# Kernel optimization log

Hardware: AMD Instinct MI355X
Metric: run time of the kernel (lower is better)

## Reference

```python
import jax, jax.numpy as jnp
import numpy as np

K = 4096      # codebook_size
D = 256       # emb_dim
DECAY = 0.99
EPS = 1e-05
BETA = 0.25


def setup_inputs() -> dict:
    key = jax.random.key(0)
    k1, k2 = jax.random.split(key)
    z_e = jax.random.normal(k1, (32, 1024, D), dtype=jnp.float32)
    codebook = jax.random.normal(k2, (K, D), dtype=jnp.float32) * 0.05
    ema_cluster_size = jnp.zeros((K,), dtype=jnp.float32)
    ema_embed_sum = jnp.zeros((K, D), dtype=jnp.float32)
    return {"z_e": z_e, "codebook": codebook,
            "ema_cluster_size": ema_cluster_size,
            "ema_embed_sum": ema_embed_sum}


def reference(z_e, codebook, ema_cluster_size, ema_embed_sum):
    lead_shape = z_e.shape[:-1]
    z = z_e.reshape(-1, D)                       # [N, D]
    N = z.shape[0]

    # squared distances: ||z||^2 + ||e||^2 - 2 z e^T   -> [N, K]
    z_sq = jnp.sum(z * z, axis=1, keepdims=True)
    e_sq = jnp.sum(codebook * codebook, axis=1)
    distances = z_sq + e_sq[None, :] - 2.0 * (z @ codebook.T)
    indices = jnp.argmin(distances, axis=1)      # [N]

    z_q = codebook[indices].reshape(z_e.shape)   # gather

    commitment = jnp.mean((z_e - jax.lax.stop_gradient(z_q)) ** 2)
    loss_vq = BETA * commitment
    z_q_st = z_e + jax.lax.stop_gradient(z_q - z_e)  # straight-through

    # EMA statistics (scatter-reduce instead of dense one-hot matmul)
    cluster_size_batch = jax.ops.segment_sum(
        jnp.ones((N,), dtype=z.dtype), indices, num_segments=K)
    embed_sum_batch = jax.ops.segment_sum(z, indices, num_segments=K)

    new_ema_cluster_size = ema_cluster_size * DECAY + (1.0 - DECAY) * cluster_size_batch
    new_ema_embed_sum = ema_embed_sum * DECAY + (1.0 - DECAY) * embed_sum_batch
    n = new_ema_cluster_size + EPS * K
    new_codebook = new_ema_embed_sum / n[:, None]

    avg_probs = cluster_size_batch / N
    perplexity = jnp.exp(-jnp.sum(avg_probs * jnp.log(avg_probs + 1e-12)))

    return (z_q_st, indices.reshape(lead_shape), loss_vq, perplexity,
            new_codebook, new_ema_cluster_size, new_ema_embed_sum)
```

## Files before the change

### kernel.cpp

```cpp
#include <hip/hip_runtime.h>
#include <hip/hip_bf16.h>
#include <math.h>

#define DIM    256
#define KCB    4096
#define NROWS  32768
#define DECAYF 0.99f
#define MARGIN 0.024f

#define OUT_ZQ   0
#define OUT_IDX  8388608
#define OUT_LOSS 8421376
#define OUT_PPL  8421377
#define OUT_CB   8421378
#define OUT_CS   9469954
#define OUT_ES   9474050

#define WS_A2      0u
#define WS_EH      33554432u
#define WS_ZSQ     35651584u
#define WS_ESQ     35782656u
#define WS_P1      35799040u
#define WS_PI      39993344u
#define WS_P2      44187648u
#define WS_IDX     48381952u
#define WS_FLIST   48513024u
#define WS_LIST2   48644096u
#define WS_BASE    48775168u
#define WS_ZERO    48791552u
#define WS_COUNTS  48791552u
#define WS_CURSOR  48807936u
#define WS_FLCNT   48824320u
#define WS_ZEROLEN 32772u

#define WS_SLOT    WS_A2
#define WS_CBT     (WS_A2 + 1048576u)

typedef __attribute__((ext_vector_type(8))) short short8;
typedef __attribute__((ext_vector_type(4))) float f32x4;

#define GLOAD(g, l) __builtin_amdgcn_global_load_lds( \
    (const __attribute__((address_space(1))) unsigned int*)(g), \
    (__attribute__((address_space(3))) unsigned int*)(l), 16, 0, 0)

__device__ __forceinline__ unsigned short f2bf(float x) {
  __hip_bfloat16 h = __float2bfloat16(x);
  return *reinterpret_cast<unsigned short*>(&h);
}

__global__ __launch_bounds__(256) void prep_all(
    const float* __restrict__ z, const float* __restrict__ cb,
    unsigned short* __restrict__ A2, unsigned short* __restrict__ EH,
    float* __restrict__ z_sq, float* __restrict__ e_sq) {
  int b = blockIdx.x;
  int lane = threadIdx.x & 63;
  const float* src;
  unsigned short* dst;
  float* sq;
  int gw;
  if (b < NROWS / 4) {
    gw = (b * 256 + threadIdx.x) >> 6;
    src = z; dst = A2; sq = z_sq;
  } else {
    gw = ((b - NROWS / 4) * 256 + threadIdx.x) >> 6;
    src = cb; dst = EH; sq = e_sq;
  }
  float4 v = *(const float4*)(src + (size_t)gw * DIM + lane * 4);
  float x[4] = {v.x, v.y, v.z, v.w};
  unsigned short h[4];
  float ss = 0.f;
#pragma unroll
  for (int i = 0; i < 4; ++i) { ss += x[i] * x[i]; h[i] = f2bf(x[i]); }
  *(ushort4*)(dst + (size_t)gw * 256 + lane * 4) =
      make_ushort4(h[0], h[1], h[2], h[3]);
#pragma unroll
  for (int off = 32; off > 0; off >>= 1) ss += __shfl_down(ss, off);
  if (lane == 0) sq[gw] = ss;
}

__global__ __launch_bounds__(256) void tp_cb(
    const float* __restrict__ cb, float* __restrict__ cbT) {
  __shared__ float tile[32][257];
  int c0 = blockIdx.x * 32;
  int t = threadIdx.x;
  int r = t >> 6, c4 = (t & 63) * 4;
#pragma unroll
  for (int i = 0; i < 8; ++i) {
    float4 v = *(const float4*)(cb + (size_t)(c0 + r + i * 4) * DIM + c4);
    tile[r + i * 4][c4 + 0] = v.x;
    tile[r + i * 4][c4 + 1] = v.y;
    tile[r + i * 4][c4 + 2] = v.z;
    tile[r + i * 4][c4 + 3] = v.w;
  }
  __syncthreads();
  int cs = (t & 7) * 4;
#pragma unroll
  for (int j = 0; j < 8; ++j) {
    int d = (t >> 3) + j * 32;
    float4 w = make_float4(tile[cs][d], tile[cs + 1][d],
                           tile[cs + 2][d], tile[cs + 3][d]);
    *(float4*)(cbT + (size_t)d * KCB + c0 + cs) = w;
  }
}

__global__ __launch_bounds__(256) void dist_mfma(
    const unsigned short* __restrict__ A2, const unsigned short* __restrict__ EH,
    const float* __restrict__ e_sq,
    float* __restrict__ p1, int* __restrict__ pi, float* __restrict__ p2) {
  __shared__ __align__(16) unsigned short sZ[3][128 * 32];
  __shared__ __align__(16) unsigned short sE[3][128 * 32];
  __shared__ float se[128];
  __shared__ float sm1[2][128];
  __shared__ int   smi[2][128];
  __shared__ float sm2[2][128];

  int wgid = blockIdx.x;
  int swz = (wgid & 7) * 1024 + (wgid >> 3);
  int rowp = swz >> 5, colp = swz & 31;
  int brow = rowp * 128, bcol = colp * 128;
  int tid = threadIdx.x;
  int lane = tid & 63, w = tid >> 6;
  int wr = w >> 1, wc = w & 1;
  int rl = lane & 15, k8 = lane >> 4;

  f32x4 acc[4][4] = {};

  int r0 = tid >> 2;
  int s_src = (tid & 3) ^ (r0 & 3) ^ ((r0 >> 2) & 3);
  const char* baseA = (const char*)A2 + (size_t)(brow + r0) * 512 + s_src * 16;
  const char* baseB = (const char*)EH + (size_t)(bcol + r0) * 512 + s_src * 16;

#define STAGE(b, ks_) do {                                                    \
    GLOAD(baseA + (ks_) * 64,         &sZ[b][tid * 8]);                       \
    GLOAD(baseA + 32768 + (ks_) * 64, &sZ[b][2048 + tid * 8]);                \
    GLOAD(baseB + (ks_) * 64,         &sE[b][tid * 8]);                       \
    GLOAD(baseB + 32768 + (ks_) * 64, &sE[b][2048 + tid * 8]);                \
  } while (0)

  if (tid < 128) se[tid] = e_sq[bcol + tid];
  STAGE(0, 0);
  STAGE(1, 1);
  __syncthreads();

#pragma unroll
  for (int ks = 0; ks < 8; ++ks) {
    if (ks >= 2 && ks < 7) { asm volatile("s_waitcnt vmcnt(4)" ::: "memory"); }
    if (ks == 7)           { asm volatile("s_waitcnt vmcnt(0)" ::: "memory"); }
    if (ks >= 1) {
      __builtin_amdgcn_sched_barrier(0);
      __builtin_amdgcn_s_barrier();
      __builtin_amdgcn_sched_barrier(0);
    }
    const unsigned short* za = sZ[ks % 3];
    const unsigned short* ea = sE[ks % 3];
    short8 ef[4], zf[4];
    int sseg = (k8 ^ (rl & 3) ^ ((rl >> 2) & 3)) * 8;
#pragma unroll
    for (int mi = 0; mi < 4; ++mi)
      ef[mi] = *(const short8*)&ea[(wr * 64 + mi * 16 + rl) * 32 + sseg];
#pragma unroll
    for (int ni = 0; ni < 4; ++ni)
      zf[ni] = *(const short8*)&za[(wc * 64 + ni * 16 + rl) * 32 + sseg];
#pragma unroll
    for (int mi = 0; mi < 4; ++mi)
#pragma unroll
      for (int ni = 0; ni < 4; ++ni)
        acc[mi][ni] = __builtin_amdgcn_mfma_f32_16x16x32_bf16(
            ef[mi], zf[ni], acc[mi][ni], 0, 0, 0);
    if (ks < 6) STAGE((ks + 2) % 3, ks + 2);
  }
#undef STAGE

  int cb0 = bcol + wr * 64 + k8 * 4;
  float e2l[4][4];
#pragma unroll
  for (int mi = 0; mi < 4; ++mi)
#pragma unroll
    for (int j = 0; j < 4; ++j)
      e2l[mi][j] = se[wr * 64 + mi * 16 + k8 * 4 + j];

#pragma unroll
  for (int ni = 0; ni < 4; ++ni) {
    float m1 = 1e30f, m2 = 1e30f; int i1 = 0;
#pragma unroll
    for (int mi = 0; mi < 4; ++mi) {
#pragma unroll
      for (int j = 0; j < 4; ++j) {
        float q = e2l[mi][j] - 2.0f * acc[mi][ni][j];
        if (q < m1) { m2 = m1; m1 = q; i1 = cb0 + mi * 16 + j; }
        else if (q < m2) m2 = q;
      }
    }
#pragma unroll
    for (int mk = 16; mk <= 32; mk <<= 1) {
      float v1 = __shfl_xor(m1, mk);
      int   vi = __shfl_xor(i1, mk);
      float v2 = __shfl_xor(m2, mk);
      float hi = fmaxf(m1, v1), lo2 = fminf(m2, v2);
      if (v1 < m1) { m1 = v1; i1 = vi; }
      else if (v1 == m1 && vi < i1) i1 = vi;
      m2 = fminf(hi, lo2);
    }
    if (k8 == 0) {
      int rowl = wc * 64 + ni * 16 + rl;
      sm1[wr][rowl] = m1; smi[wr][rowl] = i1; sm2[wr][rowl] = m2;
    }
  }
  __syncthreads();
  if (tid < 128) {
    float a1 = sm1[0][tid]; int ai = smi[0][tid]; float a2 = sm2[0][tid];
    float b1 = sm1[1][tid]; int bi = smi[1][tid]; float b2 = sm2[1][tid];
    float m1, m2; int i1;
    if (b1 < a1) { m1 = b1; i1 = bi; m2 = fminf(a1, b2); }
    else         { m1 = a1; i1 = ai; m2 = fminf(b1, a2); }
    size_t o = (size_t)colp * NROWS + (brow + tid);
    p1[o] = m1; pi[o] = i1; p2[o] = m2;
  }
}

__global__ __launch_bounds__(256) void merge_kernel(
    const float* __restrict__ p1, const int* __restrict__ pi,
    const float* __restrict__ p2, int* __restrict__ flist,
    int* __restrict__ flcnt, unsigned long long* __restrict__ slot) {
  int r = blockIdx.x * 256 + threadIdx.x;
  float m1 = 1e30f, m2 = 1e30f; int i1 = 0;
  for (int cb = 0; cb < 32; ++cb) {
    size_t o = (size_t)cb * NROWS + r;
    float v1 = p1[o]; int vi = pi[o]; float v2 = p2[o];
    float hi = fmaxf(m1, v1), lo2 = fminf(m2, v2);
    if (v1 < m1) { m1 = v1; i1 = vi; }
    else if (v1 == m1 && vi < i1) i1 = vi;
    m2 = fminf(hi, lo2);
  }
  if (m2 - m1 < MARGIN) {
    slot[r] = ~0ULL;
    int p = atomicAdd(flcnt, 1);
    flist[p] = r;
  } else {
    slot[r] = ((unsigned long long)__float_as_uint(m1) << 32) | (unsigned)i1;
  }
}

__global__ __launch_bounds__(256) void rescore_partial(
    const float* __restrict__ z, const float* __restrict__ cbT,
    const float* __restrict__ z_sq, const float* __restrict__ e_sq,
    const int* __restrict__ flist, const int* __restrict__ flcnt,
    unsigned long long* __restrict__ slot) {
  __shared__ float zs[8][256];
  __shared__ int   rid[8];
  __shared__ float zq[8];
  __shared__ unsigned long long wred[4][8];
  int t = threadIdx.x;
  int lane = t & 63, w = t >> 6;
  int cnt = *flcnt;
  int nitems = ((cnt + 7) >> 3) << 2;
  for (int it = blockIdx.x; it < nitems; it += gridDim.x) {
    int batch = it >> 2, quarter = it & 3;
    __syncthreads();
    if (t < 8) {
      int fi = batch * 8 + t;
      int rr = flist[fi < cnt ? fi : (cnt - 1)];
      rid[t] = rr; zq[t] = z_sq[rr];
    }
    __syncthreads();
    {
      int r8 = t >> 5, d0 = (t & 31) * 8;
      const float* zp = z + (size_t)rid[r8] * DIM + d0;
      *(float4*)&zs[r8][d0] = *(const float4*)(zp);
      *(float4*)&zs[r8][d0 + 4] = *(const float4*)(zp + 4);
    }
    __syncthreads();
    int cbase = quarter * 1024 + t * 4;
    float4 es4 = *(const float4*)(e_sq + cbase);
    float a0[8], a1[8], a2[8], a3[8];
#pragma unroll
    for (int r = 0; r < 8; ++r) { a0[r] = 0.f; a1[r] = 0.f; a2[r] = 0.f; a3[r] = 0.f; }
    for (int d = 0; d < DIM; ++d) {
      float4 e = *(const float4*)(cbT + (size_t)d * KCB + cbase);
#pragma unroll
      for (int r = 0; r < 8; ++r) {
        float zv = zs[r][d];
        a0[r] = fmaf(zv, e.x, a0[r]);
        a1[r] = fmaf(zv, e.y, a1[r]);
        a2[r] = fmaf(zv, e.z, a2[r]);
        a3[r] = fmaf(zv, e.w, a3[r]);
      }
    }
#pragma unroll
    for (int r = 0; r < 8; ++r) {
      float d0 = (zq[r] + es4.x) - 2.0f * a0[r];
      float d1 = (zq[r] + es4.y) - 2.0f * a1[r];
      float d2 = (zq[r] + es4.z) - 2.0f * a2[r];
      float d3 = (zq[r] + es4.w) - 2.0f * a3[r];
      float m = d0; int ci = cbase;
      if (d1 < m) { m = d1; ci = cbase + 1; }
      if (d2 < m) { m = d2; ci = cbase + 2; }
      if (d3 < m) { m = d3; ci = cbase + 3; }
      unsigned long long p =
          ((unsigned long long)__float_as_uint(m) << 32) | (unsigned)ci;
#pragma unroll
      for (int mk = 32; mk >= 1; mk >>= 1) {
        unsigned long long q = __shfl_xor(p, mk);
        if (q < p) p = q;
      }
      if (lane == 0) wred[w][r] = p;
    }
    __syncthreads();
    if (t < 8) {
      unsigned long long m = wred[0][t];
      if (wred[1][t] < m) m = wred[1][t];
      if (wred[2][t] < m) m = wred[2][t];
      if (wred[3][t] < m) m = wred[3][t];
      atomicMin(&slot[rid[t]], m);
    }
  }
}

__global__ __launch_bounds__(256) void gather_kernel(
    const float* __restrict__ z, const float* __restrict__ cb,
    const unsigned long long* __restrict__ slot, int* __restrict__ idx,
    float* __restrict__ out_idxf, float* __restrict__ out_zq,
    int* __restrict__ counts, float* __restrict__ lossp) {
  __shared__ float ls[4];
  int gw = (blockIdx.x * 256 + threadIdx.x) >> 6;
  int lane = threadIdx.x & 63;
  int w = threadIdx.x >> 6;
  int k = (int)(unsigned)(slot[gw] & 0xFFFFFFFFu);
  float4 zq = *(const float4*)(cb + (size_t)k * DIM + lane * 4);
  float4 zv = *(const float4*)(z + (size_t)gw * DIM + lane * 4);
  float4 o;
  o.x = zv.x + (zq.x - zv.x);
  o.y = zv.y + (zq.y - zv.y);
  o.z = zv.z + (zq.z - zv.z);
  o.w = zv.w + (zq.w - zv.w);
  *(float4*)(out_zq + (size_t)gw * DIM + lane * 4) = o;
  float dx = zv.x - zq.x, dy = zv.y - zq.y, dz = zv.z - zq.z, dw = zv.w - zq.w;
  float s = dx * dx + dy * dy + dz * dz + dw * dw;
#pragma unroll
  for (int off = 32; off > 0; off >>= 1) s += __shfl_down(s, off);
  if (lane == 0) {
    ls[w] = s;
    idx[gw] = k;
    out_idxf[gw] = (float)k;
    atomicAdd(&counts[k], 1);
  }
  __syncthreads();
  if (threadIdx.x == 0)
    lossp[blockIdx.x] = ls[0] + ls[1] + ls[2] + ls[3];
}

__global__ void prefix_kernel(const int* __restrict__ counts,
                              int* __restrict__ base, int* __restrict__ cursor) {
  __shared__ int part[256];
  __shared__ int pre[256];
  int t = threadIdx.x;
  int loc[16]; int s = 0;
#pragma unroll
  for (int i = 0; i < 16; ++i) { loc[i] = counts[t * 16 + i]; s += loc[i]; }
  part[t] = s;
  __syncthreads();
  if (t == 0) { int a = 0; for (int i = 0; i < 256; ++i) { pre[i] = a; a += part[i]; } }
  __syncthreads();
  int a = pre[t];
#pragma unroll
  for (int i = 0; i < 16; ++i) { base[t * 16 + i] = a; cursor[t * 16 + i] = a; a += loc[i]; }
}

__global__ void scatter_kernel(const int* __restrict__ idx,
                               int* __restrict__ cursor, int* __restrict__ list2) {
  int n = blockIdx.x * 256 + threadIdx.x;
  int k = idx[n];
  int p = atomicAdd(&cursor[k], 1);
  list2[p] = n;
}

__global__ __launch_bounds__(256) void finalize_codes(
    const float* __restrict__ ema_cs, const float* __restrict__ ema_es,
    const int* __restrict__ counts, const int* __restrict__ base,
    const int* __restrict__ list2, const float* __restrict__ z,
    float* __restrict__ out_cb, float* __restrict__ out_cs,
    float* __restrict__ out_es, const float* __restrict__ lossp,
    float* __restrict__ out_loss, float* __restrict__ out_ppl) {
  __shared__ float red[256];
  int gw = (blockIdx.x * 256 + threadIdx.x) >> 6;
  int lane = threadIdx.x & 63;
  int cnt = counts[gw], b0 = base[gw];
  float sx = 0.f, sy = 0.f, sz = 0.f, sw = 0.f;
  for (int i = 0; i < cnt; ++i) {
    int n = list2[b0 + i];
    float4 v = *(const float4*)(z + (size_t)n * DIM + lane * 4);
    sx += v.x; sy += v.y; sz += v.z; sw += v.w;
  }
  const float omd = 1.0f - DECAYF;
  float cntf = (float)cnt;
  float ncs = ema_cs[gw] * DECAYF + omd * cntf;
  float nden = ncs + 0.04096f;
  if (lane == 0) out_cs[gw] = ncs;
  size_t o = (size_t)gw * DIM + lane * 4;
  float4 em = *(const float4*)(ema_es + o);
  float nex = em.x * DECAYF + omd * sx;
  float ney = em.y * DECAYF + omd * sy;
  float nez = em.z * DECAYF + omd * sz;
  float new_ = em.w * DECAYF + omd * sw;
  *(float2*)(out_es + o) = make_float2(nex, ney);
  *(float2*)(out_es + o + 2) = make_float2(nez, new_);
  *(float2*)(out_cb + o) = make_float2(nex / nden, ney / nden);
  *(float2*)(out_cb + o + 2) = make_float2(nez / nden, new_ / nden);

  if (blockIdx.x == 0) {
    int t = threadIdx.x;
    float s = 0.f;
    for (int i = t; i < 8192; i += 256) s += lossp[i];
    float e = 0.f;
    for (int i = t; i < 4096; i += 256) {
      float p = (float)counts[i] * (1.0f / (float)NROWS);
      e -= p * logf(p + 1e-12f);
    }
    red[t] = s;
    __syncthreads();
    for (int st = 128; st > 0; st >>= 1) {
      if (t < st) red[t] += red[t + st];
      __syncthreads();
    }
    float loss_tot = red[0];
    __syncthreads();
    red[t] = e;
    __syncthreads();
    for (int st = 128; st > 0; st >>= 1) {
      if (t < st) red[t] += red[t + st];
      __syncthreads();
    }
    if (t == 0) {
      out_loss[0] = 0.25f * (loss_tot / 8388608.0f);
      out_ppl[0] = expf(red[0]);
    }
  }
}

extern "C" void kernel_launch(void* const* d_in, const int* in_sizes, int n_in,
                              void* d_out, int out_size, void* d_ws, size_t ws_size,
                              hipStream_t stream) {
  (void)in_sizes; (void)n_in; (void)out_size; (void)ws_size;
  const float* z      = (const float*)d_in[0];
  const float* cb     = (const float*)d_in[1];
  const float* ema_cs = (const float*)d_in[2];
  const float* ema_es = (const float*)d_in[3];
  float* out = (float*)d_out;
  char*  ws  = (char*)d_ws;

  unsigned short* A2 = (unsigned short*)(ws + WS_A2);
  unsigned short* EH = (unsigned short*)(ws + WS_EH);
  float* z_sq  = (float*)(ws + WS_ZSQ);
  float* e_sq  = (float*)(ws + WS_ESQ);
  float* p1    = (float*)(ws + WS_P1);
  int*   pi    = (int*)(ws + WS_PI);
  float* p2    = (float*)(ws + WS_P2);
  float* lossp = (float*)(ws + WS_P2);
  unsigned long long* slot = (unsigned long long*)(ws + WS_SLOT);
  float* cbT   = (float*)(ws + WS_CBT);
  int*   idx   = (int*)(ws + WS_IDX);
  int*   flist = (int*)(ws + WS_FLIST);
  int*   list2 = (int*)(ws + WS_LIST2);
  int*   base  = (int*)(ws + WS_BASE);
  int*   counts = (int*)(ws + WS_COUNTS);
  int*   cursor = (int*)(ws + WS_CURSOR);
  int*   flcnt  = (int*)(ws + WS_FLCNT);

  hipMemsetAsync(ws + WS_ZERO, 0, WS_ZEROLEN, stream);

  prep_all<<<NROWS / 4 + KCB / 4, 256, 0, stream>>>(z, cb, A2, EH, z_sq, e_sq);
  dist_mfma<<<(NROWS / 128) * (KCB / 128), 256, 0, stream>>>(A2, EH, e_sq,
                                                             p1, pi, p2);
  tp_cb<<<KCB / 32, 256, 0, stream>>>(cb, cbT);
  merge_kernel<<<NROWS / 256, 256, 0, stream>>>(p1, pi, p2, flist, flcnt,
                                                slot);
  rescore_partial<<<2048, 256, 0, stream>>>(z, cbT, z_sq, e_sq, flist, flcnt,
                                            slot);
  gather_kernel<<<NROWS / 4, 256, 0, stream>>>(z, cb, slot, idx,
                                               out + OUT_IDX, out + OUT_ZQ,
                                               counts, lossp);
  prefix_kernel<<<1, 256, 0, stream>>>(counts, base, cursor);
  scatter_kernel<<<NROWS / 256, 256, 0, stream>>>(idx, cursor, list2);
  finalize_codes<<<KCB / 4, 256, 0, stream>>>(ema_cs, ema_es, counts, base,
                                              list2, z, out + OUT_CB,
                                              out + OUT_CS, out + OUT_ES,
                                              lossp, out + OUT_LOSS,
                                              out + OUT_PPL);
}
```

Before: 258.6 us.

## Restage dist GEMM into two four-buffer bulk phases and fuse transpose with merge

The distance GEMM's three-buffer software pipeline, with per-k-step barriers and partial waitcnts, is replaced by two phases. Each phase loads four K-slices into a four-deep LDS buffer, waits for all of them, then runs four MFMA steps back to back. Separately, the codebook transpose kernel is merged into the merge kernel as extra blocks, which removes one launch. The GEMM change cuts barriers but drops load/compute overlap and doubles LDS use, which may lower occupancy.

```diff
diff --git a/kernel.cpp b/kernel.cpp
--- a/kernel.cpp
+++ b/kernel.cpp
@@ -78,37 +78,12 @@
   if (lane == 0) sq[gw] = ss;
 }
 
-__global__ __launch_bounds__(256) void tp_cb(
-    const float* __restrict__ cb, float* __restrict__ cbT) {
-  __shared__ float tile[32][257];
-  int c0 = blockIdx.x * 32;
-  int t = threadIdx.x;
-  int r = t >> 6, c4 = (t & 63) * 4;
-#pragma unroll
-  for (int i = 0; i < 8; ++i) {
-    float4 v = *(const float4*)(cb + (size_t)(c0 + r + i * 4) * DIM + c4);
-    tile[r + i * 4][c4 + 0] = v.x;
-    tile[r + i * 4][c4 + 1] = v.y;
-    tile[r + i * 4][c4 + 2] = v.z;
-    tile[r + i * 4][c4 + 3] = v.w;
-  }
-  __syncthreads();
-  int cs = (t & 7) * 4;
-#pragma unroll
-  for (int j = 0; j < 8; ++j) {
-    int d = (t >> 3) + j * 32;
-    float4 w = make_float4(tile[cs][d], tile[cs + 1][d],
-                           tile[cs + 2][d], tile[cs + 3][d]);
-    *(float4*)(cbT + (size_t)d * KCB + c0 + cs) = w;
-  }
-}
-
 __global__ __launch_bounds__(256) void dist_mfma(
     const unsigned short* __restrict__ A2, const unsigned short* __restrict__ EH,
     const float* __restrict__ e_sq,
     float* __restrict__ p1, int* __restrict__ pi, float* __restrict__ p2) {
-  __shared__ __align__(16) unsigned short sZ[3][128 * 32];
-  __shared__ __align__(16) unsigned short sE[3][128 * 32];
+  __shared__ __align__(16) unsigned short sZ[4][128 * 32];
+  __shared__ __align__(16) unsigned short sE[4][128 * 32];
   __shared__ float se[128];
   __shared__ float sm1[2][128];
   __shared__ int   smi[2][128];
@@ -137,38 +112,40 @@
     GLOAD(baseB + 32768 + (ks_) * 64, &sE[b][2048 + tid * 8]);                \
   } while (0)
 
+#define COMPUTE(bi) do {                                                      \
+    const unsigned short* za = sZ[bi];                                        \
+    const unsigned short* ea = sE[bi];                                        \
+    short8 ef[4], zf[4];                                                      \
+    _Pragma("unroll")                                                         \
+    for (int mi = 0; mi < 4; ++mi)                                            \
+      ef[mi] = *(const short8*)&ea[(wr * 64 + mi * 16 + rl) * 32 + sseg];     \
+    _Pragma("unroll")                                                         \
+    for (int ni = 0; ni < 4; ++ni)                                            \
+      zf[ni] = *(const short8*)&za[(wc * 64 + ni * 16 + rl) * 32 + sseg];     \
+    _Pragma("unroll")                                                         \
+    for (int mi = 0; mi < 4; ++mi)                                            \
+      _Pragma("unroll")                                                       \
+      for (int ni = 0; ni < 4; ++ni)                                          \
+        acc[mi][ni] = __builtin_amdgcn_mfma_f32_16x16x32_bf16(                \
+            ef[mi], zf[ni], acc[mi][ni], 0, 0, 0);                            \
+  } while (0)
+
+  int sseg = (k8 ^ (rl & 3) ^ ((rl >> 2) & 3)) * 8;
+
   if (tid < 128) se[tid] = e_sq[bcol + tid];
-  STAGE(0, 0);
-  STAGE(1, 1);
-  __syncthreads();
-
-#pragma unroll
-  for (int ks = 0; ks < 8; ++ks) {
-    if (ks >= 2 && ks < 7) { asm volatile("s_waitcnt vmcnt(4)" ::: "memory"); }
-    if (ks == 7)           { asm volatile("s_waitcnt vmcnt(0)" ::: "memory"); }
-    if (ks >= 1) {
-      __builtin_amdgcn_sched_barrier(0);
-      __builtin_amdgcn_s_barrier();
-      __builtin_amdgcn_sched_barrier(0);
-    }
-    const unsigned short* za = sZ[ks % 3];
-    const unsigned short* ea = sE[ks % 3];
-    short8 ef[4], zf[4];
-    int sseg = (k8 ^ (rl & 3) ^ ((rl >> 2) & 3)) * 8;
-#pragma unroll
-    for (int mi = 0; mi < 4; ++mi)
-      ef[mi] = *(const short8*)&ea[(wr * 64 + mi * 16 + rl) * 32 + sseg];
-#pragma unroll
-    for (int ni = 0; ni < 4; ++ni)
-      zf[ni] = *(const short8*)&za[(wc * 64 + ni * 16 + rl) * 32 + sseg];
-#pragma unroll
-    for (int mi = 0; mi < 4; ++mi)
-#pragma unroll
-      for (int ni = 0; ni < 4; ++ni)
-        acc[mi][ni] = __builtin_amdgcn_mfma_f32_16x16x32_bf16(
-            ef[mi], zf[ni], acc[mi][ni], 0, 0, 0);
-    if (ks < 6) STAGE((ks + 2) % 3, ks + 2);
-  }
+  STAGE(0, 0); STAGE(1, 1); STAGE(2, 2); STAGE(3, 3);
+  asm volatile("s_waitcnt vmcnt(0)" ::: "memory");
+  __syncthreads();
+
+  COMPUTE(0); COMPUTE(1); COMPUTE(2); COMPUTE(3);
+  __syncthreads();
+
+  STAGE(0, 4); STAGE(1, 5); STAGE(2, 6); STAGE(3, 7);
+  asm volatile("s_waitcnt vmcnt(0)" ::: "memory");
+  __syncthreads();
+
+  COMPUTE(0); COMPUTE(1); COMPUTE(2); COMPUTE(3);
+#undef COMPUTE
 #undef STAGE
 
   int cb0 = bcol + wr * 64 + k8 * 4;
@@ -218,26 +195,52 @@
   }
 }
 
-__global__ __launch_bounds__(256) void merge_kernel(
+__global__ __launch_bounds__(256) void merge_tp(
     const float* __restrict__ p1, const int* __restrict__ pi,
     const float* __restrict__ p2, int* __restrict__ flist,
-    int* __restrict__ flcnt, unsigned long long* __restrict__ slot) {
-  int r = blockIdx.x * 256 + threadIdx.x;
-  float m1 = 1e30f, m2 = 1e30f; int i1 = 0;
-  for (int cb = 0; cb < 32; ++cb) {
-    size_t o = (size_t)cb * NROWS + r;
-    float v1 = p1[o]; int vi = pi[o]; float v2 = p2[o];
-    float hi = fmaxf(m1, v1), lo2 = fminf(m2, v2);
-    if (v1 < m1) { m1 = v1; i1 = vi; }
-    else if (v1 == m1 && vi < i1) i1 = vi;
-    m2 = fminf(hi, lo2);
-  }
-  if (m2 - m1 < MARGIN) {
-    slot[r] = ~0ULL;
-    int p = atomicAdd(flcnt, 1);
-    flist[p] = r;
+    int* __restrict__ flcnt, unsigned long long* __restrict__ slot,
+    const float* __restrict__ cb, float* __restrict__ cbT) {
+  __shared__ float tile[32][257];
+  int b = blockIdx.x;
+  int t = threadIdx.x;
+  if (b < NROWS / 256) {
+    int r = b * 256 + t;
+    float m1 = 1e30f, m2 = 1e30f; int i1 = 0;
+    for (int cbk = 0; cbk < 32; ++cbk) {
+      size_t o = (size_t)cbk * NROWS + r;
+      float v1 = p1[o]; int vi = pi[o]; float v2 = p2[o];
+      float hi = fmaxf(m1, v1), lo2 = fminf(m2, v2);
+      if (v1 < m1) { m1 = v1; i1 = vi; }
+      else if (v1 == m1 && vi < i1) i1 = vi;
+      m2 = fminf(hi, lo2);
+    }
+    if (m2 - m1 < MARGIN) {
+      slot[r] = ~0ULL;
+      int p = atomicAdd(flcnt, 1);
+      flist[p] = r;
+    } else {
+      slot[r] = ((unsigned long long)__float_as_uint(m1) << 32) | (unsigned)i1;
+    }
   } else {
-    slot[r] = ((unsigned long long)__float_as_uint(m1) << 32) | (unsigned)i1;
+    int c0 = (b - NROWS / 256) * 32;
+    int r = t >> 6, c4 = (t & 63) * 4;
+#pragma unroll
+    for (int i = 0; i < 8; ++i) {
+      float4 v = *(const float4*)(cb + (size_t)(c0 + r + i * 4) * DIM + c4);
+      tile[r + i * 4][c4 + 0] = v.x;
+      tile[r + i * 4][c4 + 1] = v.y;
+      tile[r + i * 4][c4 + 2] = v.z;
+      tile[r + i * 4][c4 + 3] = v.w;
+    }
+    __syncthreads();
+    int cs = (t & 7) * 4;
+#pragma unroll
+    for (int j = 0; j < 8; ++j) {
+      int d = (t >> 3) + j * 32;
+      float4 wv = make_float4(tile[cs][d], tile[cs + 1][d],
+                              tile[cs + 2][d], tile[cs + 3][d]);
+      *(float4*)(cbT + (size_t)d * KCB + c0 + cs) = wv;
+    }
   }
 }
 
@@ -471,9 +474,8 @@
   prep_all<<<NROWS / 4 + KCB / 4, 256, 0, stream>>>(z, cb, A2, EH, z_sq, e_sq);
   dist_mfma<<<(NROWS / 128) * (KCB / 128), 256, 0, stream>>>(A2, EH, e_sq,
                                                              p1, pi, p2);
-  tp_cb<<<KCB / 32, 256, 0, stream>>>(cb, cbT);
-  merge_kernel<<<NROWS / 256, 256, 0, stream>>>(p1, pi, p2, flist, flcnt,
-                                                slot);
+  merge_tp<<<NROWS / 256 + KCB / 32, 256, 0, stream>>>(p1, pi, p2, flist,
+                                                       flcnt, slot, cb, cbT);
   rescore_partial<<<2048, 256, 0, stream>>>(z, cbT, z_sq, e_sq, flist, flcnt,
                                             slot);
   gather_kernel<<<NROWS / 4, 256, 0, stream>>>(z, cb, slot, idx,
```

Result: slower. 274.3 us (+6.1%).
